# Kernel optimization log

Hardware: AMD Instinct MI355X
Metric: run time of the kernel (lower is better)

Reference implementation:

```python
import jax, jax.numpy as jnp
import numpy as np

B, T, C = 4, 2048, 1024
N_HEAD = 16
HEAD_SIZE = C // N_HEAD


def setup_inputs() -> dict:
    key = jax.random.key(0)
    ks = jax.random.split(key, 9)
    std = 0.02
    return {
        "x": jax.random.normal(ks[0], (B, T, C), dtype=jnp.float32),
        "Wk": jax.random.normal(ks[1], (C, C), dtype=jnp.float32) * std,
        "bk": jnp.zeros((C,), dtype=jnp.float32),
        "Wq": jax.random.normal(ks[2], (C, C), dtype=jnp.float32) * std,
        "bq": jnp.zeros((C,), dtype=jnp.float32),
        "Wv": jax.random.normal(ks[3], (C, C), dtype=jnp.float32) * std,
        "bv": jnp.zeros((C,), dtype=jnp.float32),
        "Wo": jax.random.normal(ks[4], (C, C), dtype=jnp.float32) * std,
        "bo": jnp.zeros((C,), dtype=jnp.float32),
    }


def reference(x, Wk, bk, Wq, bq, Wv, bv, Wo, bo):
    # QKV projections -> (B, T, H, D)
    k = (x @ Wk + bk).reshape(B, T, N_HEAD, HEAD_SIZE)
    q = (x @ Wq + bq).reshape(B, T, N_HEAD, HEAD_SIZE)
    v = (x @ Wv + bv).reshape(B, T, N_HEAD, HEAD_SIZE)
    # Scaled causal attention scores: (B, H, T, T)
    scale = 1.0 / jnp.sqrt(jnp.asarray(HEAD_SIZE, dtype=x.dtype))
    scores = jnp.einsum("bqhd,bkhd->bhqk", q, k) * scale
    causal = jnp.tril(jnp.ones((T, T), dtype=bool))
    scores = jnp.where(causal, scores, jnp.asarray(-1e10, dtype=x.dtype))
    probs = jax.nn.softmax(scores, axis=-1)
    # Weighted values -> (B, T, H, D) -> (B, T, C)
    y = jnp.einsum("bhqk,bkhd->bqhd", probs, v).reshape(B, T, C)
    # Output projection (dropout rates are 0 / deterministic)
    return y @ Wo + bo
```

## Files before the change

### kernel.cpp

```cpp
#include <hip/hip_runtime.h>
#include <hip/hip_bf16.h>

typedef unsigned short ushort_t;
typedef __attribute__((ext_vector_type(8))) short short8;
typedef __attribute__((ext_vector_type(4))) float floatx4;

#define BATCH 4
#define SEQ   2048
#define CH    1024
#define NHEAD 16
#define HSZ   64
#define MROWS (BATCH * SEQ)

#define GLD16(gptr, lptr) \
    __builtin_amdgcn_global_load_lds((const __attribute__((address_space(1))) unsigned int*)(gptr), \
                                     (__attribute__((address_space(3))) unsigned int*)(lptr), 16, 0, 0)

__device__ inline ushort_t f2b(float f) {
    __hip_bfloat16 h = __float2bfloat16(f);
    return *(ushort_t*)&h;
}
__device__ inline float b2f(ushort_t u) {
    return __bfloat162float(*(__hip_bfloat16*)&u);
}

__device__ __forceinline__ float fast_exp2(float x) {
#if __has_builtin(__builtin_amdgcn_exp2f)
    return __builtin_amdgcn_exp2f(x);
#else
    float r; asm("v_exp_f32 %0, %1" : "=v"(r) : "v"(x)); return r;
#endif
}

__global__ void detect_dtype(const ushort_t* __restrict__ x, int* __restrict__ flag) {
    int cnt = 0;
    #pragma unroll
    for (int i = 0; i < 8; i++) {
        const int e = (x[2 * (threadIdx.x * 8 + i)] >> 7) & 0xFF;
        const unsigned long long m = __ballot(e >= 100 && e <= 140);
        cnt += (int)__popcll(m);
    }
    if (threadIdx.x == 0) *flag = (cnt >= 400) ? 1 : 0;
}

__global__ __launch_bounds__(256) void convert_wt4(const void* w0, const void* w1,
                                                   const void* w2, const void* w3,
                                                   ushort_t* o0, ushort_t* o1,
                                                   ushort_t* o2, ushort_t* o3,
                                                   const int* __restrict__ flag) {
    __shared__ ushort_t tile[32][33];
    const void* in = (blockIdx.z == 0) ? w0 : (blockIdx.z == 1) ? w1 : (blockIdx.z == 2) ? w2 : w3;
    ushort_t*  out = (blockIdx.z == 0) ? o0 : (blockIdx.z == 1) ? o1 : (blockIdx.z == 2) ? o2 : o3;
    const int am = *flag;
    const int bx = blockIdx.x * 32, by = blockIdx.y * 32;
    const int tx = threadIdx.x & 31, ty = threadIdx.x >> 5;
    #pragma unroll
    for (int r = ty; r < 32; r += 8) {
        const size_t idx = (size_t)(by + r) * CH + bx + tx;
        tile[r][tx] = am ? ((const ushort_t*)in)[idx] : f2b(((const float*)in)[idx]);
    }
    __syncthreads();
    #pragma unroll
    for (int r = ty; r < 32; r += 8)
        out[(size_t)(bx + r) * CH + by + tx] = tile[tx][r];
}

__global__ void convert_bias4(const void* b0, const void* b1, const void* b2, const void* b3,
                              ushort_t* __restrict__ out, const int* __restrict__ flag) {
    const int i = blockIdx.x * 256 + threadIdx.x;
    const int m = i >> 10, idx = i & 1023;
    const void* in = (m == 0) ? b0 : (m == 1) ? b1 : (m == 2) ? b2 : b3;
    out[i] = (*flag) ? ((const ushort_t*)in)[idx] : f2b(((const float*)in)[idx]);
}

__global__ __launch_bounds__(256) void convert_x(const void* __restrict__ in,
                                                 ushort_t* __restrict__ out,
                                                 const int* __restrict__ flag) {
    const int i = (blockIdx.x * 256 + threadIdx.x) * 8;
    if (*flag) {
        *(float4*)&out[i] = *(const float4*)&((const ushort_t*)in)[i];
    } else {
        const float* p = (const float*)in + i;
        float4 f0 = *(const float4*)p;
        float4 f1 = *(const float4*)(p + 4);
        ushort_t t[8] = {f2b(f0.x), f2b(f0.y), f2b(f0.z), f2b(f0.w),
                         f2b(f1.x), f2b(f1.y), f2b(f1.z), f2b(f1.w)};
        *(float4*)&out[i] = *(const float4*)t;
    }
}

__device__ __forceinline__ void pipe256x128(const ushort_t* __restrict__ A,
                                            const ushort_t* __restrict__ Bt,
                                            int row0, int col0,
                                            ushort_t* __restrict__ As,
                                            ushort_t* __restrict__ Bs,
                                            floatx4 acc[4][4], int tid) {
    const int lane = tid & 63, wave = tid >> 6;
    const int lane15 = lane & 15, quad = lane >> 4;
    const int s7 = lane15 & 7;
    const int wm = wave >> 1, wn = wave & 1;
    const int lrow = lane >> 3, lu = lane & 7, gu = lu ^ lrow;
    const int brow = tid >> 3, bu = tid & 7, bgu = bu ^ (brow & 7);

    auto stage_part = [&](int buf, int tt, int h) {
        ushort_t* Ad = As + buf * (256 * 64) + (h * 128 + wave * 16 + lrow) * 64 + lu * 8;
        const ushort_t* Asrc = A + (size_t)(row0 + h * 128 + wave * 16 + lrow) * CH + tt * 64 + gu * 8;
        GLD16(Asrc, Ad);
        GLD16(Asrc + 8 * CH, Ad + 8 * 64);
        ushort_t* Bd = Bs + buf * (128 * 64) + (h * 64 + brow) * 64 + bu * 8;
        const ushort_t* Bsrc = Bt + (size_t)(col0 + h * 64 + brow) * CH + tt * 64 + bgu * 8;
        GLD16(Bsrc, Bd);
    };

    stage_part(0, 0, 0); stage_part(0, 0, 1);
    stage_part(1, 1, 0); stage_part(1, 1, 1);
    asm volatile("s_waitcnt vmcnt(6)" ::: "memory");
    __builtin_amdgcn_s_barrier();

    int buf = 0;
    for (int t = 0; t < 16; ++t) {
        const ushort_t* Ab = As + buf * (256 * 64) + (wm * 64) * 64;
        const ushort_t* Bb = Bs + buf * (128 * 64) + (wn * 64) * 64;
        int bnext = buf + 2; if (bnext >= 3) bnext -= 3;
        const bool pf = (t + 2 < 16);
        #pragma unroll
        for (int kk = 0; kk < 2; ++kk) {
            short8 af[4], bfr[4];
            #pragma unroll
            for (int i = 0; i < 4; i++)
                af[i] = *(const short8*)&Ab[(i * 16 + lane15) * 64 + (((kk * 4 + quad) ^ s7) * 8)];
            #pragma unroll
            for (int j = 0; j < 4; j++)
                bfr[j] = *(const short8*)&Bb[(j * 16 + lane15) * 64 + (((kk * 4 + quad) ^ s7) * 8)];
            if (pf) stage_part(bnext, t + 2, kk);
            __builtin_amdgcn_s_barrier();
            __builtin_amdgcn_s_setprio(1);
            #pragma unroll
            for (int i = 0; i < 4; i++)
                #pragma unroll
                for (int j = 0; j < 4; j++)
                    acc[i][j] = __builtin_amdgcn_mfma_f32_16x16x32_bf16(af[i], bfr[j], acc[i][j], 0, 0, 0);
            __builtin_amdgcn_s_setprio(0);
            if (kk == 1 && t < 15) {
                if (pf) asm volatile("s_waitcnt vmcnt(6)" ::: "memory");
                else    asm volatile("s_waitcnt vmcnt(0)" ::: "memory");
            }
            __builtin_amdgcn_s_barrier();
        }
        buf = (buf == 2) ? 0 : buf + 1;
    }
}

__global__ __launch_bounds__(512) void gemm_qkv8(const ushort_t* __restrict__ A,
                                                 const ushort_t* __restrict__ Bt,
                                                 const ushort_t* __restrict__ bias,
                                                 ushort_t* __restrict__ Qb,
                                                 ushort_t* __restrict__ Kb,
                                                 ushort_t* __restrict__ Vt,
                                                 float qscale) {
    __shared__ __align__(16) ushort_t As[3 * 256 * 64];
    __shared__ __align__(16) ushort_t Bs[3 * 128 * 64];
    const int tid = threadIdx.x;
    const int lane = tid & 63, wave = tid >> 6;
    const int lane15 = lane & 15, quad = lane >> 4;
    const int wm = wave >> 1, wn = wave & 1;
    const int bid = blockIdx.x;
    const int bidl = (bid & 7) * 96 + (bid >> 3);
    const int rowblk = bidl / 24, colblk = bidl - rowblk * 24;
    const int row0 = rowblk * 256, col0 = colblk * 128;
    const int seg = col0 >> 10;

    floatx4 acc[4][4];
    #pragma unroll
    for (int i = 0; i < 4; i++)
        #pragma unroll
        for (int j = 0; j < 4; j++) acc[i][j] = {0.f, 0.f, 0.f, 0.f};

    pipe256x128(A, Bt, row0, col0, As, Bs, acc, tid);

    #pragma unroll
    for (int j = 0; j < 4; j++) {
        const int col = col0 + wn * 64 + j * 16 + lane15;
        const float bv = b2f(bias[col]);
        #pragma unroll
        for (int i = 0; i < 4; i++) {
            const int rowb = row0 + wm * 64 + i * 16 + quad * 4;
            if (seg == 0) {
                #pragma unroll
                for (int r = 0; r < 4; r++)
                    Qb[(size_t)(rowb + r) * CH + col] = f2b((acc[i][j][r] + bv) * qscale);
            } else if (seg == 1) {
                const int c = col - 1024;
                #pragma unroll
                for (int r = 0; r < 4; r++)
                    Kb[(size_t)(rowb + r) * CH + c] = f2b(acc[i][j][r] + bv);
            } else {
                const int c = col - 2048;
                ushort_t pk[4];
                #pragma unroll
                for (int r = 0; r < 4; r++) pk[r] = f2b(acc[i][j][r] + bv);
                const int bb = rowb >> 11, tc = rowb & 2047;
                *(uint2*)&Vt[((size_t)bb * 1024 + c) * 2048 + tc] = *(const uint2*)pk;
            }
        }
    }
}

__global__ __launch_bounds__(512) void gemm_bt8(const ushort_t* __restrict__ A,
                                                const ushort_t* __restrict__ Bt,
                                                const ushort_t* __restrict__ bias,
                                                void* __restrict__ Out,
                                                const int* __restrict__ oflag) {
    __shared__ __align__(16) ushort_t As[3 * 256 * 64];
    __shared__ __align__(16) ushort_t Bs[3 * 128 * 64];
    const int om = *oflag;
    const int tid = threadIdx.x;
    const int lane = tid & 63, wave = tid >> 6;
    const int lane15 = lane & 15, quad = lane >> 4;
    const int wm = wave >> 1, wn = wave & 1;
    const int bid = blockIdx.x;
    const int bidl = (bid & 7) * 32 + (bid >> 3);
    const int rowblk = bidl >> 3, colblk = bidl & 7;
    const int row0 = rowblk * 256, col0 = colblk * 128;

    floatx4 acc[4][4];
    #pragma unroll
    for (int i = 0; i < 4; i++)
        #pragma unroll
        for (int j = 0; j < 4; j++) acc[i][j] = {0.f, 0.f, 0.f, 0.f};

    pipe256x128(A, Bt, row0, col0, As, Bs, acc, tid);

    #pragma unroll
    for (int j = 0; j < 4; j++) {
        const int col = col0 + wn * 64 + j * 16 + lane15;
        const float bv = b2f(bias[col]);
        #pragma unroll
        for (int i = 0; i < 4; i++) {
            const int rowb = row0 + wm * 64 + i * 16 + quad * 4;
            #pragma unroll
            for (int r = 0; r < 4; r++) {
                const float val = acc[i][j][r] + bv;
                const size_t idx = (size_t)(rowb + r) * CH + col;
                if (om) ((ushort_t*)Out)[idx] = f2b(val);
                else    ((float*)Out)[idx] = val;
            }
        }
    }
}

__global__ __launch_bounds__(256) void attn_fwd(ushort_t* __restrict__ QY,
                                                const ushort_t* __restrict__ K,
                                                const ushort_t* __restrict__ Vt) {
    __shared__ __align__(16) ushort_t Ks[2][64 * 64];
    __shared__ __align__(16) ushort_t Vs[2][64 * 64];
    __shared__ __align__(16) ushort_t Ps[4 * 32 * 64];
    const int tid = threadIdx.x;
    const int lane = tid & 63, wave = tid >> 6;
    const int lane15 = lane & 15, quad = lane >> 4;
    const int sw = lane15 & 7;
    const int bid = blockIdx.x;
    const int hb = bid & 63, qslot = bid >> 6;
    const int qb = 15 - qslot;
    const int h = hb & 15, b = hb >> 4;
    const int q0 = qb * 128;
    const size_t baseR = (size_t)b * SEQ * CH + h * HSZ;
    const size_t baseV = ((size_t)b * 1024 + h * HSZ) * SEQ;
    const int rg = lane >> 3, cg = (lane & 7) ^ rg;
    const int psBase = wave * 2048;

    short8 qf[2][2];
    #pragma unroll
    for (int mm = 0; mm < 2; mm++) {
        const ushort_t* qp = QY + baseR + (size_t)(q0 + wave * 32 + mm * 16 + lane15) * CH + quad * 8;
        qf[mm][0] = *(const short8*)qp;
        qf[mm][1] = *(const short8*)(qp + 32);
    }
    const short8 kOnes = (short8)(short)0x3F80;

    floatx4 o[2][5];
    #pragma unroll
    for (int mm = 0; mm < 2; mm++)
        #pragma unroll
        for (int j = 0; j < 5; j++) o[mm][j] = {0.f, 0.f, 0.f, 0.f};

    const int nkt = 2 * qb + 2;
    #pragma unroll
    for (int l = wave; l < 8; l += 4) {
        GLD16(K  + baseR + (size_t)(l * 8 + rg) * CH + cg * 8, &Ks[0][l * 512]);
        GLD16(Vt + baseV + (size_t)(l * 8 + rg) * SEQ + cg * 8, &Vs[0][l * 512]);
    }

    for (int kt = 0; kt < nkt; kt++) {
        __syncthreads();
        const int cur = kt & 1;
        if (kt + 1 < nkt) {
            const int kv1 = (kt + 1) * 64, nb = cur ^ 1;
            #pragma unroll
            for (int l = wave; l < 8; l += 4) {
                GLD16(K  + baseR + (size_t)(kv1 + l * 8 + rg) * CH + cg * 8, &Ks[nb][l * 512]);
                GLD16(Vt + baseV + (size_t)(l * 8 + rg) * SEQ + kv1 + cg * 8, &Vs[nb][l * 512]);
            }
        }
        const int kv0 = kt * 64;
        const int masked = (kt >= 2 * qb);

        short8 kf[4][2];
        #pragma unroll
        for (int g = 0; g < 4; g++) {
            kf[g][0] = *(const short8*)&Ks[cur][(g * 16 + lane15) * 64 + ((quad ^ sw) * 8)];
            kf[g][1] = *(const short8*)&Ks[cur][(g * 16 + lane15) * 64 + (((quad + 4) ^ sw) * 8)];
        }

        #pragma unroll
        for (int mm = 0; mm < 2; mm++) {
            const int qrow = q0 + wave * 32 + mm * 16 + lane15;
            const int rowOff = psBase + (mm * 16 + lane15) * 64;
            #pragma unroll
            for (int g = 0; g < 4; g++) {
                floatx4 z = {0.f, 0.f, 0.f, 0.f};
                z = __builtin_amdgcn_mfma_f32_16x16x32_bf16(kf[g][0], qf[mm][0], z, 0, 0, 0);
                z = __builtin_amdgcn_mfma_f32_16x16x32_bf16(kf[g][1], qf[mm][1], z, 0, 0, 0);
                if (masked) {
                    #pragma unroll
                    for (int r = 0; r < 4; r++) {
                        const int col = kv0 + g * 16 + quad * 4 + r;
                        z[r] = (col <= qrow) ? z[r] : -1e30f;
                    }
                }
                const float p0 = fast_exp2(z[0]), p1 = fast_exp2(z[1]);
                const float p2 = fast_exp2(z[2]), p3 = fast_exp2(z[3]);
                unsigned int lo, hi;
                asm("v_cvt_pk_bf16_f32 %0, %1, %2" : "=v"(lo) : "v"(p0), "v"(p1));
                asm("v_cvt_pk_bf16_f32 %0, %1, %2" : "=v"(hi) : "v"(p2), "v"(p3));
                uint2 w; w.x = lo; w.y = hi;
                *(uint2*)&Ps[rowOff + (((g * 4 + quad) ^ lane15) * 4)] = w;
            }
        }

        #pragma unroll
        for (int kk = 0; kk < 2; kk++) {
            #pragma unroll
            for (int mm = 0; mm < 2; mm++) {
                const int rowOff = psBase + (mm * 16 + lane15) * 64;
                const int c0 = kk * 8 + quad * 2;
                short8 a;
                ((uint2*)&a)[0] = *(const uint2*)&Ps[rowOff + (((c0    ) ^ lane15) * 4)];
                ((uint2*)&a)[1] = *(const uint2*)&Ps[rowOff + (((c0 + 1) ^ lane15) * 4)];
                #pragma unroll
                for (int jn = 0; jn < 4; jn++) {
                    short8 bb = *(const short8*)&Vs[cur][(jn * 16 + lane15) * 64 + (((kk * 4 + quad) ^ sw) * 8)];
                    o[mm][jn] = __builtin_amdgcn_mfma_f32_16x16x32_bf16(a, bb, o[mm][jn], 0, 0, 0);
                }
                o[mm][4] = __builtin_amdgcn_mfma_f32_16x16x32_bf16(a, kOnes, o[mm][4], 0, 0, 0);
            }
        }
    }

    #pragma unroll
    for (int mm = 0; mm < 2; mm++)
        #pragma unroll
        for (int r = 0; r < 4; r++) {
            const int qrow = q0 + wave * 32 + mm * 16 + quad * 4 + r;
            const float rinv = 1.0f / fmaxf(o[mm][4][r], 1e-30f);
            #pragma unroll
            for (int jn = 0; jn < 4; jn++)
                QY[baseR + (size_t)qrow * CH + jn * 16 + lane15] = f2b(o[mm][jn][r] * rinv);
        }
}

extern "C" void kernel_launch(void* const* d_in, const int* in_sizes, int n_in,
                              void* d_out, int out_size, void* d_ws, size_t ws_size,
                              hipStream_t stream) {
    const void* x  = d_in[0];
    const void* Wk = d_in[1];
    const void* bk = d_in[2];
    const void* Wq = d_in[3];
    const void* bq = d_in[4];
    const void* Wv = d_in[5];
    const void* bv = d_in[6];
    const void* Wo = d_in[7];
    const void* bo = d_in[8];

    ushort_t* ws    = (ushort_t*)d_ws;
    int*      flag  = (int*)d_ws;
    ushort_t* biasC = ws + 2048;
    ushort_t* WqkvT = ws + 32768;
    ushort_t* WoT   = WqkvT + 3u * (1u << 20);
    ushort_t* xb    = ws + 4227072;
    ushort_t* Qb    = ws + 12615680;
    ushort_t* Kb    = (ushort_t*)d_out;
    ushort_t* VtB   = Kb + (size_t)MROWS * CH;

    detect_dtype<<<1, 64, 0, stream>>>((const ushort_t*)x, flag);

    dim3 tgrid(32, 32, 4);
    convert_wt4<<<tgrid, 256, 0, stream>>>(Wq, Wk, Wv, Wo,
                                           WqkvT, WqkvT + (1u << 20), WqkvT + 2u * (1u << 20), WoT, flag);
    convert_bias4<<<16, 256, 0, stream>>>(bq, bk, bv, bo, biasC, flag);
    convert_x<<<MROWS * CH / (256 * 8), 256, 0, stream>>>(x, xb, flag);

    gemm_qkv8<<<dim3(768), 512, 0, stream>>>(xb, WqkvT, biasC, Qb, Kb, VtB, 0.1803368801f);

    attn_fwd<<<dim3(1024), 256, 0, stream>>>(Qb, Kb, VtB);

    gemm_bt8<<<dim3(256), 512, 0, stream>>>(Qb, WoT, biasC + 3072, d_out, flag);
}
```

Before: 243.8 us.

## Enlarge QKV GEMM tile to 256x256 with BK=32 triple-buffered pipeline

Replaces the 256x128 QKV projection kernel with a 256x256 output tile per block, using K-steps of 32 with a new swizzled LDS layout and staging split into two halves interleaved with the MFMA phases. Each wave now holds an 8x4 grid of accumulators, and the grid drops from 768 to 384 blocks. The aim is higher arithmetic intensity and less redundant global/LDS traffic per FLOP. In exchange it roughly doubles accumulator registers, which may lower occupancy, and it leaves fewer blocks to spread across CUs.

New measurement: 258.5 us. 1.06x slower.

```diff
diff --git a/kernel.cpp b/kernel.cpp
--- a/kernel.cpp
+++ b/kernel.cpp
@@ -89,6 +89,117 @@
     }
 }
 
+__global__ __launch_bounds__(512) void gemm_qkv9(const ushort_t* __restrict__ A,
+                                                 const ushort_t* __restrict__ Bt,
+                                                 const ushort_t* __restrict__ bias,
+                                                 ushort_t* __restrict__ Qb,
+                                                 ushort_t* __restrict__ Kb,
+                                                 ushort_t* __restrict__ Vt,
+                                                 float qscale) {
+    __shared__ __align__(16) ushort_t As[3][256 * 32];
+    __shared__ __align__(16) ushort_t Bs[3][256 * 32];
+    const int tid = threadIdx.x;
+    const int lane = tid & 63, wave = tid >> 6;
+    const int lane15 = lane & 15, quad = lane >> 4;
+    const int wm = wave >> 2, wn = wave & 3;
+    const int k15 = (lane15 >> 1) & 3;
+    const int srow = tid >> 2;
+    const int sulog = (tid & 3) ^ ((tid >> 3) & 3);
+    const int bid = blockIdx.x;
+    const int bidl = (bid & 7) * 48 + (bid >> 3);
+    const int rowblk = bidl / 12, colblk = bidl - rowblk * 12;
+    const int row0 = rowblk * 256, col0 = colblk * 256;
+    const int seg = col0 >> 10;
+
+    floatx4 acc[8][4];
+    #pragma unroll
+    for (int m = 0; m < 8; m++)
+        #pragma unroll
+        for (int n = 0; n < 4; n++) acc[m][n] = {0.f, 0.f, 0.f, 0.f};
+
+    auto stage_h = [&](int bf, int tt, int h) {
+        const int kof = tt * 32 + sulog * 8;
+        const int r = h * 128 + srow;
+        GLD16(A  + (size_t)(row0 + r) * CH + kof, &As[bf][r * 32 + (tid & 3) * 8]);
+        GLD16(Bt + (size_t)(col0 + r) * CH + kof, &Bs[bf][r * 32 + (tid & 3) * 8]);
+    };
+
+    stage_h(0, 0, 0); stage_h(0, 0, 1);
+    stage_h(1, 1, 0); stage_h(1, 1, 1);
+    asm volatile("s_waitcnt vmcnt(4)" ::: "memory");
+    __builtin_amdgcn_s_barrier();
+
+    int buf = 0;
+    for (int t = 0; t < 32; ++t) {
+        const ushort_t* Ab = As[buf];
+        const ushort_t* Bb = Bs[buf];
+        int bnext = buf + 2; if (bnext >= 3) bnext -= 3;
+        const bool pf = (t + 2 < 32);
+        short8 af[4], bfr[4];
+        #pragma unroll
+        for (int m = 0; m < 4; m++)
+            af[m] = *(const short8*)&Ab[(wm * 128 + m * 16 + lane15) * 32 + ((quad ^ k15) * 8)];
+        #pragma unroll
+        for (int n = 0; n < 4; n++)
+            bfr[n] = *(const short8*)&Bb[(wn * 64 + n * 16 + lane15) * 32 + ((quad ^ k15) * 8)];
+        if (pf) stage_h(bnext, t + 2, 0);
+        __builtin_amdgcn_s_barrier();
+        __builtin_amdgcn_s_setprio(1);
+        #pragma unroll
+        for (int m = 0; m < 4; m++)
+            #pragma unroll
+            for (int n = 0; n < 4; n++)
+                acc[m][n] = __builtin_amdgcn_mfma_f32_16x16x32_bf16(af[m], bfr[n], acc[m][n], 0, 0, 0);
+        __builtin_amdgcn_s_setprio(0);
+        __builtin_amdgcn_s_barrier();
+        #pragma unroll
+        for (int m = 0; m < 4; m++)
+            af[m] = *(const short8*)&Ab[(wm * 128 + (m + 4) * 16 + lane15) * 32 + ((quad ^ k15) * 8)];
+        if (pf) stage_h(bnext, t + 2, 1);
+        __builtin_amdgcn_s_barrier();
+        __builtin_amdgcn_s_setprio(1);
+        #pragma unroll
+        for (int m = 0; m < 4; m++)
+            #pragma unroll
+            for (int n = 0; n < 4; n++)
+                acc[m + 4][n] = __builtin_amdgcn_mfma_f32_16x16x32_bf16(af[m], bfr[n], acc[m + 4][n], 0, 0, 0);
+        __builtin_amdgcn_s_setprio(0);
+        if (t < 31) {
+            if (pf) asm volatile("s_waitcnt vmcnt(4)" ::: "memory");
+            else    asm volatile("s_waitcnt vmcnt(0)" ::: "memory");
+        }
+        __builtin_amdgcn_s_barrier();
+        buf = (buf == 2) ? 0 : buf + 1;
+    }
+
+    #pragma unroll
+    for (int n = 0; n < 4; n++) {
+        const int col = col0 + wn * 64 + n * 16 + lane15;
+        const float bv = b2f(bias[col]);
+        #pragma unroll
+        for (int m = 0; m < 8; m++) {
+            const int rowb = row0 + wm * 128 + m * 16 + quad * 4;
+            if (seg == 0) {
+                #pragma unroll
+                for (int r = 0; r < 4; r++)
+                    Qb[(size_t)(rowb + r) * CH + col] = f2b((acc[m][n][r] + bv) * qscale);
+            } else if (seg == 1) {
+                const int c = col - 1024;
+                #pragma unroll
+                for (int r = 0; r < 4; r++)
+                    Kb[(size_t)(rowb + r) * CH + c] = f2b(acc[m][n][r] + bv);
+            } else {
+                const int c = col - 2048;
+                ushort_t pk[4];
+                #pragma unroll
+                for (int r = 0; r < 4; r++) pk[r] = f2b(acc[m][n][r] + bv);
+                const int bb = rowb >> 11, tc = rowb & 2047;
+                *(uint2*)&Vt[((size_t)bb * 1024 + c) * 2048 + tc] = *(const uint2*)pk;
+            }
+        }
+    }
+}
+
 __device__ __forceinline__ void pipe256x128(const ushort_t* __restrict__ A,
                                             const ushort_t* __restrict__ Bt,
                                             int row0, int col0,
@@ -148,61 +259,6 @@
             __builtin_amdgcn_s_barrier();
         }
         buf = (buf == 2) ? 0 : buf + 1;
-    }
-}
-
-__global__ __launch_bounds__(512) void gemm_qkv8(const ushort_t* __restrict__ A,
-                                                 const ushort_t* __restrict__ Bt,
-                                                 const ushort_t* __restrict__ bias,
-                                                 ushort_t* __restrict__ Qb,
-                                                 ushort_t* __restrict__ Kb,
-                                                 ushort_t* __restrict__ Vt,
-                                                 float qscale) {
-    __shared__ __align__(16) ushort_t As[3 * 256 * 64];
-    __shared__ __align__(16) ushort_t Bs[3 * 128 * 64];
-    const int tid = threadIdx.x;
-    const int lane = tid & 63, wave = tid >> 6;
-    const int lane15 = lane & 15, quad = lane >> 4;
-    const int wm = wave >> 1, wn = wave & 1;
-    const int bid = blockIdx.x;
-    const int bidl = (bid & 7) * 96 + (bid >> 3);
-    const int rowblk = bidl / 24, colblk = bidl - rowblk * 24;
-    const int row0 = rowblk * 256, col0 = colblk * 128;
-    const int seg = col0 >> 10;
-
-    floatx4 acc[4][4];
-    #pragma unroll
-    for (int i = 0; i < 4; i++)
-        #pragma unroll
-        for (int j = 0; j < 4; j++) acc[i][j] = {0.f, 0.f, 0.f, 0.f};
-
-    pipe256x128(A, Bt, row0, col0, As, Bs, acc, tid);
-
-    #pragma unroll
-    for (int j = 0; j < 4; j++) {
-        const int col = col0 + wn * 64 + j * 16 + lane15;
-        const float bv = b2f(bias[col]);
-        #pragma unroll
-        for (int i = 0; i < 4; i++) {
-            const int rowb = row0 + wm * 64 + i * 16 + quad * 4;
-            if (seg == 0) {
-                #pragma unroll
-                for (int r = 0; r < 4; r++)
-                    Qb[(size_t)(rowb + r) * CH + col] = f2b((acc[i][j][r] + bv) * qscale);
-            } else if (seg == 1) {
-                const int c = col - 1024;
-                #pragma unroll
-                for (int r = 0; r < 4; r++)
-                    Kb[(size_t)(rowb + r) * CH + c] = f2b(acc[i][j][r] + bv);
-            } else {
-                const int c = col - 2048;
-                ushort_t pk[4];
-                #pragma unroll
-                for (int r = 0; r < 4; r++) pk[r] = f2b(acc[i][j][r] + bv);
-                const int bb = rowb >> 11, tc = rowb & 2047;
-                *(uint2*)&Vt[((size_t)bb * 1024 + c) * 2048 + tc] = *(const uint2*)pk;
-            }
-        }
     }
 }
 
@@ -400,7 +456,7 @@
     convert_bias4<<<16, 256, 0, stream>>>(bq, bk, bv, bo, biasC, flag);
     convert_x<<<MROWS * CH / (256 * 8), 256, 0, stream>>>(x, xb, flag);
 
-    gemm_qkv8<<<dim3(768), 512, 0, stream>>>(xb, WqkvT, biasC, Qb, Kb, VtB, 0.1803368801f);
+    gemm_qkv9<<<dim3(384), 512, 0, stream>>>(xb, WqkvT, biasC, Qb, Kb, VtB, 0.1803368801f);
 
     attn_fwd<<<dim3(1024), 256, 0, stream>>>(Qb, Kb, VtB);
 
```

## Fuse dtype detection and input conversions into one prep kernel; batch GEMM prefetch

Applied to the files above, without the earlier changes.

Merges the dtype-detect, weight transpose/convert, bias convert and x convert kernels into a single launch. Each block recomputes the dtype flag from a smaller sample of x, which removes three launches and the serial dependency on the flag. Separately, the GEMM pipeline now issues both halves of the next-stage prefetch in the first k-substep instead of spreading them across two, which changes load/compute interleaving. The smaller detection sample (256 values instead of 512) could change how the flag is decided for borderline inputs.

Result: slower. 249.8 us (+2.4%).

```diff
diff --git a/kernel.cpp b/kernel.cpp
--- a/kernel.cpp
+++ b/kernel.cpp
@@ -32,60 +32,59 @@
 #endif
 }
 
-__global__ void detect_dtype(const ushort_t* __restrict__ x, int* __restrict__ flag) {
-    int cnt = 0;
-    #pragma unroll
-    for (int i = 0; i < 8; i++) {
-        const int e = (x[2 * (threadIdx.x * 8 + i)] >> 7) & 0xFF;
+__global__ __launch_bounds__(256) void prep_all(const void* __restrict__ x,
+        const void* __restrict__ w0, const void* __restrict__ w1,
+        const void* __restrict__ w2, const void* __restrict__ w3,
+        const void* __restrict__ b0, const void* __restrict__ b1,
+        const void* __restrict__ b2, const void* __restrict__ b3,
+        ushort_t* __restrict__ WqkvT, ushort_t* __restrict__ WoT,
+        ushort_t* __restrict__ biasC, ushort_t* __restrict__ xb,
+        int* __restrict__ flagOut) {
+    __shared__ int cnts[4];
+    __shared__ ushort_t tile[32][33];
+    const int tid = threadIdx.x;
+    {
+        const int e = (((const ushort_t*)x)[2 * tid] >> 7) & 0xFF;
         const unsigned long long m = __ballot(e >= 100 && e <= 140);
-        cnt += (int)__popcll(m);
-    }
-    if (threadIdx.x == 0) *flag = (cnt >= 400) ? 1 : 0;
-}
-
-__global__ __launch_bounds__(256) void convert_wt4(const void* w0, const void* w1,
-                                                   const void* w2, const void* w3,
-                                                   ushort_t* o0, ushort_t* o1,
-                                                   ushort_t* o2, ushort_t* o3,
-                                                   const int* __restrict__ flag) {
-    __shared__ ushort_t tile[32][33];
-    const void* in = (blockIdx.z == 0) ? w0 : (blockIdx.z == 1) ? w1 : (blockIdx.z == 2) ? w2 : w3;
-    ushort_t*  out = (blockIdx.z == 0) ? o0 : (blockIdx.z == 1) ? o1 : (blockIdx.z == 2) ? o2 : o3;
-    const int am = *flag;
-    const int bx = blockIdx.x * 32, by = blockIdx.y * 32;
-    const int tx = threadIdx.x & 31, ty = threadIdx.x >> 5;
-    #pragma unroll
-    for (int r = ty; r < 32; r += 8) {
-        const size_t idx = (size_t)(by + r) * CH + bx + tx;
-        tile[r][tx] = am ? ((const ushort_t*)in)[idx] : f2b(((const float*)in)[idx]);
+        if ((tid & 63) == 0) cnts[tid >> 6] = (int)__popcll(m);
     }
     __syncthreads();
-    #pragma unroll
-    for (int r = ty; r < 32; r += 8)
-        out[(size_t)(bx + r) * CH + by + tx] = tile[tx][r];
-}
-
-__global__ void convert_bias4(const void* b0, const void* b1, const void* b2, const void* b3,
-                              ushort_t* __restrict__ out, const int* __restrict__ flag) {
-    const int i = blockIdx.x * 256 + threadIdx.x;
-    const int m = i >> 10, idx = i & 1023;
-    const void* in = (m == 0) ? b0 : (m == 1) ? b1 : (m == 2) ? b2 : b3;
-    out[i] = (*flag) ? ((const ushort_t*)in)[idx] : f2b(((const float*)in)[idx]);
-}
-
-__global__ __launch_bounds__(256) void convert_x(const void* __restrict__ in,
-                                                 ushort_t* __restrict__ out,
-                                                 const int* __restrict__ flag) {
-    const int i = (blockIdx.x * 256 + threadIdx.x) * 8;
-    if (*flag) {
-        *(float4*)&out[i] = *(const float4*)&((const ushort_t*)in)[i];
+    const int am = (cnts[0] + cnts[1] + cnts[2] + cnts[3]) >= 128 ? 1 : 0;
+    const int bid = blockIdx.x;
+    if (bid < 4096) {
+        const int z = bid >> 10, b10 = bid & 1023;
+        const void* in = (z == 0) ? w0 : (z == 1) ? w1 : (z == 2) ? w2 : w3;
+        ushort_t*  out = (z == 0) ? WqkvT : (z == 1) ? (WqkvT + (1u << 20))
+                       : (z == 2) ? (WqkvT + 2u * (1u << 20)) : WoT;
+        const int bx = (b10 & 31) * 32, by = (b10 >> 5) * 32;
+        const int tx = tid & 31, ty = tid >> 5;
+        #pragma unroll
+        for (int r = ty; r < 32; r += 8) {
+            const size_t idx = (size_t)(by + r) * CH + bx + tx;
+            tile[r][tx] = am ? ((const ushort_t*)in)[idx] : f2b(((const float*)in)[idx]);
+        }
+        __syncthreads();
+        #pragma unroll
+        for (int r = ty; r < 32; r += 8)
+            out[(size_t)(bx + r) * CH + by + tx] = tile[tx][r];
+    } else if (bid < 4112) {
+        const int i = (bid - 4096) * 256 + tid;
+        const int m = i >> 10, idx = i & 1023;
+        const void* in = (m == 0) ? b0 : (m == 1) ? b1 : (m == 2) ? b2 : b3;
+        biasC[i] = am ? ((const ushort_t*)in)[idx] : f2b(((const float*)in)[idx]);
+        if (i == 0) *flagOut = am;
     } else {
-        const float* p = (const float*)in + i;
-        float4 f0 = *(const float4*)p;
-        float4 f1 = *(const float4*)(p + 4);
-        ushort_t t[8] = {f2b(f0.x), f2b(f0.y), f2b(f0.z), f2b(f0.w),
-                         f2b(f1.x), f2b(f1.y), f2b(f1.z), f2b(f1.w)};
-        *(float4*)&out[i] = *(const float4*)t;
+        const int i = ((bid - 4112) * 256 + tid) * 8;
+        if (am) {
+            *(float4*)&xb[i] = *(const float4*)&((const ushort_t*)x)[i];
+        } else {
+            const float* p = (const float*)x + i;
+            float4 f0 = *(const float4*)p;
+            float4 f1 = *(const float4*)(p + 4);
+            ushort_t t[8] = {f2b(f0.x), f2b(f0.y), f2b(f0.z), f2b(f0.w),
+                             f2b(f1.x), f2b(f1.y), f2b(f1.z), f2b(f1.w)};
+            *(float4*)&xb[i] = *(const float4*)t;
+        }
     }
 }
 
@@ -132,7 +131,10 @@
             #pragma unroll
             for (int j = 0; j < 4; j++)
                 bfr[j] = *(const short8*)&Bb[(j * 16 + lane15) * 64 + (((kk * 4 + quad) ^ s7) * 8)];
-            if (pf) stage_part(bnext, t + 2, kk);
+            if (kk == 0 && pf) {
+                stage_part(bnext, t + 2, 0);
+                stage_part(bnext, t + 2, 1);
+            }
             __builtin_amdgcn_s_barrier();
             __builtin_amdgcn_s_setprio(1);
             #pragma unroll
@@ -392,13 +394,8 @@
     ushort_t* Kb    = (ushort_t*)d_out;
     ushort_t* VtB   = Kb + (size_t)MROWS * CH;
 
-    detect_dtype<<<1, 64, 0, stream>>>((const ushort_t*)x, flag);
-
-    dim3 tgrid(32, 32, 4);
-    convert_wt4<<<tgrid, 256, 0, stream>>>(Wq, Wk, Wv, Wo,
-                                           WqkvT, WqkvT + (1u << 20), WqkvT + 2u * (1u << 20), WoT, flag);
-    convert_bias4<<<16, 256, 0, stream>>>(bq, bk, bv, bo, biasC, flag);
-    convert_x<<<MROWS * CH / (256 * 8), 256, 0, stream>>>(x, xb, flag);
+    prep_all<<<dim3(8208), 256, 0, stream>>>(x, Wq, Wk, Wv, Wo, bq, bk, bv, bo,
+                                             WqkvT, WoT, biasC, xb, flag);
 
     gemm_qkv8<<<dim3(768), 512, 0, stream>>>(xb, WqkvT, biasC, Qb, Kb, VtB, 0.1803368801f);
 
```
